# Optimization experiments

Measured on AMD Instinct MI355X. Metric: run time of the kernel, lower is better.

## Reference

```python
import jax, jax.numpy as jnp
import numpy as np

MIN_DISTANCE = 1.0  # default forward arg of the torch module


def setup_inputs() -> dict:
    key = jax.random.key(0)
    k1, k2 = jax.random.split(key)
    B, N = 4, 4096
    coords = jax.random.normal(k1, (B, N, 3), dtype=jnp.float32) * 5.0
    steric_radii = jax.random.uniform(k2, (B, N), dtype=jnp.float32)
    return {"coords": coords, "steric_radii": steric_radii}


def reference(coords, steric_radii):
    # coords: [B,N,3], steric_radii: [B,N]
    diff = coords[:, :, None, :] - coords[:, None, :, :]          # [B,N,N,3]
    d2 = jnp.sum(diff * diff, axis=-1)                             # [B,N,N]
    # safe sqrt: exact 0 on the diagonal (matches torch.cdist), no NaN grads
    pairwise = jnp.where(d2 > 0, jnp.sqrt(jnp.where(d2 > 0, d2, 1.0)), 0.0)
    sr = steric_radii[:, :, None] + steric_radii[:, None, :]       # [B,N,N]
    target = jnp.maximum(MIN_DISTANCE, sr)
    penalty = jax.nn.relu(target - pairwise)[..., None]            # [B,N,N,1]
    direction = jnp.clip(diff, -1.0, 1.0)                          # [B,N,N,3]
    adjustment = jnp.mean(penalty * direction, axis=2)             # [B,N,3]
    return coords + 0.1 * adjustment
```

## Files before the change

### kernel.cpp

```cpp
#include <hip/hip_runtime.h>

#define BB 4
#define NN 4096
#define TPB 1024
#define STREAMS 32
#define JPS (NN / STREAMS)
#define GRP 4

#if __has_builtin(__builtin_amdgcn_sqrtf)
  #define FAST_SQRT __builtin_amdgcn_sqrtf
#else
  #define FAST_SQRT sqrtf
#endif

__device__ __forceinline__ float clip1(float x) {
    return fminf(fmaxf(x, -1.0f), 1.0f);
}

__global__ __launch_bounds__(TPB, 8) void ncp_one(
    const float* __restrict__ coords,
    const float* __restrict__ radii,
    float* __restrict__ out)
{
    __shared__ __align__(16) char smem[65536];
    float4* pts = (float4*)smem;
    float*  red = (float*)smem;

    const int b = blockIdx.z;
    const int ibase = blockIdx.x * 32;

    for (int p = threadIdx.x; p < NN; p += TPB) {
        const int g = b * NN + p;
        pts[p] = make_float4(coords[3 * g + 0], coords[3 * g + 1],
                             coords[3 * g + 2], radii[g]);
    }
    __syncthreads();

    const int l = threadIdx.x & 63;
    const int li = l & 31;
    const int half = l >> 5;
    const int w = threadIdx.x >> 6;
    const int stream = w * 2 + half;
    const int i = ibase + li;

    const float4 me = pts[i];
    const float xi = me.x, yi = me.y, zi = me.z, ri = me.w;
    const int jbase = stream * JPS;

    float ax = 0.0f, ay = 0.0f, az = 0.0f;

    for (int k0 = 0; k0 < JPS; k0 += GRP) {
        float4 c[GRP];
        #pragma unroll
        for (int g = 0; g < GRP; ++g)
            c[g] = pts[jbase + k0 + g];
        #pragma unroll
        for (int g = 0; g < GRP; ++g) {
            const float dx = xi - c[g].x;
            const float dy = yi - c[g].y;
            const float dz = zi - c[g].z;
            const float d2 = fmaf(dx, dx, fmaf(dy, dy, dz * dz));
            if (__any(d2 < 4.0f)) {
                const float dist = FAST_SQRT(d2);
                const float tgt  = fmaxf(1.0f, ri + c[g].w);
                const float p    = fmaxf(tgt - dist, 0.0f);
                ax = fmaf(p, clip1(dx), ax);
                ay = fmaf(p, clip1(dy), ay);
                az = fmaf(p, clip1(dz), az);
            }
        }
    }

    __syncthreads();
    const int rb = (stream * 32 + li) * 3;
    red[rb + 0] = ax;
    red[rb + 1] = ay;
    red[rb + 2] = az;
    __syncthreads();

    if (threadIdx.x < 96) {
        const int ii = threadIdx.x / 3;
        const int comp = threadIdx.x % 3;
        float acc = 0.0f;
        #pragma unroll
        for (int s = 0; s < STREAMS; ++s)
            acc += red[(s * 32 + ii) * 3 + comp];
        const int o = (b * NN + ibase + ii) * 3 + comp;
        out[o] = fmaf(0.1f / (float)NN, acc, coords[o]);
    }
}

extern "C" void kernel_launch(void* const* d_in, const int* in_sizes, int n_in,
                              void* d_out, int out_size, void* d_ws, size_t ws_size,
                              hipStream_t stream) {
    const float* coords = (const float*)d_in[0];
    const float* radii  = (const float*)d_in[1];
    float* out = (float*)d_out;
    (void)d_ws; (void)ws_size;

    ncp_one<<<dim3(NN / 32, 1, BB), TPB, 0, stream>>>(coords, radii, out);
}
```

Before: 73.71 us.

## Process two query points per thread with expanded-norm distance test

Each thread now accumulates forces for two i-points, so every shared-memory j-point load is reused twice and half as many blocks reload the point table. The squared distance is computed as |j|^2 - 2 i·j compared against a precomputed 4 - |i|^2 threshold, with |j|^2 shared across both i-points. Launch bounds occupancy hint is lowered to 4. The expanded form risks cancellation error in d2 near small distances.

After: 74.82 us. Within noise of the previous version (+1.5%).

```diff
diff --git a/kernel.cpp b/kernel.cpp
--- a/kernel.cpp
+++ b/kernel.cpp
@@ -3,6 +3,7 @@
 #define BB 4
 #define NN 4096
 #define TPB 1024
+#define IBL 64
 #define STREAMS 32
 #define JPS (NN / STREAMS)
 #define GRP 4
@@ -17,7 +18,7 @@
     return fminf(fmaxf(x, -1.0f), 1.0f);
 }
 
-__global__ __launch_bounds__(TPB, 8) void ncp_one(
+__global__ __launch_bounds__(TPB, 4) void ncp_one(
     const float* __restrict__ coords,
     const float* __restrict__ radii,
     float* __restrict__ out)
@@ -27,7 +28,7 @@
     float*  red = (float*)smem;
 
     const int b = blockIdx.z;
-    const int ibase = blockIdx.x * 32;
+    const int ibase = blockIdx.x * IBL;
 
     for (int p = threadIdx.x; p < NN; p += TPB) {
         const int g = b * NN + p;
@@ -41,13 +42,20 @@
     const int half = l >> 5;
     const int w = threadIdx.x >> 6;
     const int stream = w * 2 + half;
-    const int i = ibase + li;
-
-    const float4 me = pts[i];
-    const float xi = me.x, yi = me.y, zi = me.z, ri = me.w;
     const int jbase = stream * JPS;
 
-    float ax = 0.0f, ay = 0.0f, az = 0.0f;
+    const float4 me0 = pts[ibase + li];
+    const float4 me1 = pts[ibase + 32 + li];
+    const float m2x0 = -2.0f * me0.x, m2y0 = -2.0f * me0.y, m2z0 = -2.0f * me0.z;
+    const float m2x1 = -2.0f * me1.x, m2y1 = -2.0f * me1.y, m2z1 = -2.0f * me1.z;
+    const float ri0 = me0.w, ri1 = me1.w;
+    const float n20 = fmaf(me0.z, me0.z, fmaf(me0.y, me0.y, me0.x * me0.x));
+    const float n21 = fmaf(me1.z, me1.z, fmaf(me1.y, me1.y, me1.x * me1.x));
+    const float thr0 = 4.0f - n20;
+    const float thr1 = 4.0f - n21;
+
+    float ax0 = 0.0f, ay0 = 0.0f, az0 = 0.0f;
+    float ax1 = 0.0f, ay1 = 0.0f, az1 = 0.0f;
 
     for (int k0 = 0; k0 < JPS; k0 += GRP) {
         float4 c[GRP];
@@ -56,36 +64,54 @@
             c[g] = pts[jbase + k0 + g];
         #pragma unroll
         for (int g = 0; g < GRP; ++g) {
-            const float dx = xi - c[g].x;
-            const float dy = yi - c[g].y;
-            const float dz = zi - c[g].z;
-            const float d2 = fmaf(dx, dx, fmaf(dy, dy, dz * dz));
-            if (__any(d2 < 4.0f)) {
-                const float dist = FAST_SQRT(d2);
-                const float tgt  = fmaxf(1.0f, ri + c[g].w);
+            const float nj = fmaf(c[g].z, c[g].z,
+                             fmaf(c[g].y, c[g].y, c[g].x * c[g].x));
+            const float sd0 = fmaf(m2z0, c[g].z,
+                              fmaf(m2y0, c[g].y, fmaf(m2x0, c[g].x, nj)));
+            const float sd1 = fmaf(m2z1, c[g].z,
+                              fmaf(m2y1, c[g].y, fmaf(m2x1, c[g].x, nj)));
+            if (__any(sd0 < thr0)) {
+                const float dist = FAST_SQRT(fmaxf(sd0 + n20, 0.0f));
+                const float tgt  = fmaxf(1.0f, ri0 + c[g].w);
                 const float p    = fmaxf(tgt - dist, 0.0f);
-                ax = fmaf(p, clip1(dx), ax);
-                ay = fmaf(p, clip1(dy), ay);
-                az = fmaf(p, clip1(dz), az);
+                const float dx   = fmaf(-0.5f, m2x0, -c[g].x);
+                const float dy   = fmaf(-0.5f, m2y0, -c[g].y);
+                const float dz   = fmaf(-0.5f, m2z0, -c[g].z);
+                ax0 = fmaf(p, clip1(dx), ax0);
+                ay0 = fmaf(p, clip1(dy), ay0);
+                az0 = fmaf(p, clip1(dz), az0);
+            }
+            if (__any(sd1 < thr1)) {
+                const float dist = FAST_SQRT(fmaxf(sd1 + n21, 0.0f));
+                const float tgt  = fmaxf(1.0f, ri1 + c[g].w);
+                const float p    = fmaxf(tgt - dist, 0.0f);
+                const float dx   = fmaf(-0.5f, m2x1, -c[g].x);
+                const float dy   = fmaf(-0.5f, m2y1, -c[g].y);
+                const float dz   = fmaf(-0.5f, m2z1, -c[g].z);
+                ax1 = fmaf(p, clip1(dx), ax1);
+                ay1 = fmaf(p, clip1(dy), ay1);
+                az1 = fmaf(p, clip1(dz), az1);
             }
         }
     }
 
     __syncthreads();
-    const int rb = (stream * 32 + li) * 3;
-    red[rb + 0] = ax;
-    red[rb + 1] = ay;
-    red[rb + 2] = az;
+    {
+        const int r0 = (stream * IBL + li) * 3;
+        const int r1 = (stream * IBL + 32 + li) * 3;
+        red[r0 + 0] = ax0; red[r0 + 1] = ay0; red[r0 + 2] = az0;
+        red[r1 + 0] = ax1; red[r1 + 1] = ay1; red[r1 + 2] = az1;
+    }
     __syncthreads();
 
-    if (threadIdx.x < 96) {
+    if (threadIdx.x < IBL * 3) {
         const int ii = threadIdx.x / 3;
         const int comp = threadIdx.x % 3;
         float acc = 0.0f;
         #pragma unroll
         for (int s = 0; s < STREAMS; ++s)
-            acc += red[(s * 32 + ii) * 3 + comp];
-        const int o = (b * NN + ibase + ii) * 3 + comp;
+            acc += red[(s * IBL + ii) * 3 + comp];
+        const int o = (b * NN + ibase) * 3 + threadIdx.x;
         out[o] = fmaf(0.1f / (float)NN, acc, coords[o]);
     }
 }
@@ -98,5 +124,5 @@
     float* out = (float*)d_out;
     (void)d_ws; (void)ws_size;
 
-    ncp_one<<<dim3(NN / 32, 1, BB), TPB, 0, stream>>>(coords, radii, out);
+    ncp_one<<<dim3(NN / IBL, 1, BB), TPB, 0, stream>>>(coords, radii, out);
 }
```
